# Kernel optimization log

Hardware: AMD Instinct MI355X
Metric: run time of the kernel (lower is better)

Reference implementation:

```python
import jax, jax.numpy as jnp
import numpy as np

D_MODEL = 512
N_HEADS = 8
DEPTH = D_MODEL // N_HEADS
NEG_INF = -1000000000.0


def setup_inputs() -> dict:
    key = jax.random.key(0)
    ks = jax.random.split(key, 12)
    B, S = 4, 2048
    scale = 0.02
    return {
        "Q": jax.random.normal(ks[0], (B, S, D_MODEL), jnp.float32),
        "K": jax.random.normal(ks[1], (B, S, D_MODEL), jnp.float32),
        "V": jax.random.normal(ks[2], (B, S, D_MODEL), jnp.float32),
        "mask": jax.random.randint(ks[3], (B, S, S), 0, 2, jnp.int32),
        "Wq": jax.random.normal(ks[4], (D_MODEL, D_MODEL), jnp.float32) * scale,
        "bq": jnp.zeros((D_MODEL,), jnp.float32),
        "Wk": jax.random.normal(ks[5], (D_MODEL, D_MODEL), jnp.float32) * scale,
        "bk": jnp.zeros((D_MODEL,), jnp.float32),
        "Wv": jax.random.normal(ks[6], (D_MODEL, D_MODEL), jnp.float32) * scale,
        "bv": jnp.zeros((D_MODEL,), jnp.float32),
        "Wo": jax.random.normal(ks[7], (D_MODEL, D_MODEL), jnp.float32) * scale,
        "bo": jnp.zeros((D_MODEL,), jnp.float32),
    }


def _split_heads(x, B):
    # [B, S, d_model] -> [B, H, S, depth]
    S = x.shape[1]
    return x.reshape(B, S, N_HEADS, DEPTH).transpose(0, 2, 1, 3)


def reference(Q, K, V, mask, Wq, bq, Wk, bk, Wv, bv, Wo, bo):
    B, S, _ = Q.shape
    q = _split_heads(Q @ Wq + bq, B)  # [B,H,S,d]
    k = _split_heads(K @ Wk + bk, B)
    v = _split_heads(V @ Wv + bv, B)
    scores = jnp.einsum("bhqd,bhkd->bhqk", q, k) / jnp.sqrt(
        jnp.asarray(DEPTH, jnp.float32))
    m = mask[:, None, :, :]  # broadcast over heads: [B,1,S,S]
    scores = jnp.where(m == 0, jnp.asarray(NEG_INF, scores.dtype), scores)
    attn = jax.nn.softmax(scores, axis=-1)
    ctx = jnp.einsum("bhqk,bhkd->bhqd", attn, v)
    ctx = ctx.transpose(0, 2, 1, 3).reshape(B, S, D_MODEL)
    return ctx @ Wo + bo
```

## Files before the change

kernel.cpp:

```cpp
#include <hip/hip_runtime.h>
#include <hip/hip_bf16.h>
#include <stdint.h>

typedef unsigned short u16;
typedef unsigned int u32;
typedef unsigned long long u64;
using bf16x8 = __attribute__((ext_vector_type(8))) __bf16;
using f32x4  = __attribute__((ext_vector_type(4))) float;
using f32x16 = __attribute__((ext_vector_type(16))) float;

static constexpr int B_ = 4, H_ = 8, S_ = 2048, D_ = 64, DM_ = 512;
#define QSCALE 0.1803368801111601f

__device__ __forceinline__ u16 f2b(float f) {
  u32 u = __float_as_uint(f);
  u = (u + 0x7FFFu + ((u >> 16) & 1u)) >> 16;
  return (u16)u;
}

__device__ __forceinline__ u32 cvtpk_bf16(float a, float b) {
  u32 r;
  asm("v_cvt_pk_bf16_f32 %0, %1, %2" : "=v"(r) : "v"(a), "v"(b));
  return r;
}
__device__ __forceinline__ void plswap(u32& a, u32& b) {
  asm("v_permlane32_swap_b32 %0, %1" : "+v"(a), "+v"(b));
}
__device__ __forceinline__ void gload16(const void* g, void* lds) {
  __builtin_amdgcn_global_load_lds(
      (const __attribute__((address_space(1))) u32*)g,
      (__attribute__((address_space(3))) u32*)lds, 16, 0, 0);
}
#if __has_builtin(__builtin_amdgcn_exp2f)
__device__ __forceinline__ float exp2fast(float x) { return __builtin_amdgcn_exp2f(x); }
#else
__device__ __forceinline__ float exp2fast(float x) {
  float r;
  asm("v_exp_f32 %0, %1" : "=v"(r) : "v"(x));
  return r;
}
#endif

__global__ __launch_bounds__(256) void prep_w_kernel(
    const float* __restrict__ Wq, const float* __restrict__ Wk,
    const float* __restrict__ Wv, const float* __restrict__ Wo,
    u16* __restrict__ Wtq, u16* __restrict__ Wtk, u16* __restrict__ Wtv, u16* __restrict__ Wto) {
  __shared__ float tile[32][33];
  const int z = blockIdx.z;
  const float* W = z == 0 ? Wq : z == 1 ? Wk : z == 2 ? Wv : Wo;
  u16* Wt       = z == 0 ? Wtq : z == 1 ? Wtk : z == 2 ? Wtv : Wto;
  const int k0 = blockIdx.x * 32, n0 = blockIdx.y * 32;
  const int t = threadIdx.x;
  {
    const int kl = t >> 3, nl4 = (t & 7) * 4;
    float4 v = *(const float4*)(W + (size_t)(k0 + kl) * DM_ + n0 + nl4);
    tile[kl][nl4 + 0] = v.x; tile[kl][nl4 + 1] = v.y;
    tile[kl][nl4 + 2] = v.z; tile[kl][nl4 + 3] = v.w;
  }
  __syncthreads();
  {
    const int nl = t >> 3, kl4 = (t & 7) * 4;
    ushort4 o;
    o.x = f2b(tile[kl4 + 0][nl]); o.y = f2b(tile[kl4 + 1][nl]);
    o.z = f2b(tile[kl4 + 2][nl]); o.w = f2b(tile[kl4 + 3][nl]);
    *(ushort4*)(Wt + (size_t)(n0 + nl) * DM_ + k0 + kl4) = o;
  }
}

__global__ void pack_mask_kernel(const int* __restrict__ mask, u32* __restrict__ bits) {
  int i = blockIdx.x * blockDim.x + threadIdx.x;
  unsigned long long bal = __ballot(mask[i] != 0);
  int lane = threadIdx.x & 63;
  if (lane == 0)       bits[i >> 5] = (u32)bal;
  else if (lane == 32) bits[i >> 5] = (u32)(bal >> 32);
}

__global__ __launch_bounds__(256) void gemm_qkv_kernel(
    const float* __restrict__ Qf, const float* __restrict__ Kf, const float* __restrict__ Vf,
    const u16* __restrict__ Wtq, const u16* __restrict__ Wtk, const u16* __restrict__ Wtv,
    const float* __restrict__ bq, const float* __restrict__ bk, const float* __restrict__ bv,
    u16* __restrict__ qp, u16* __restrict__ kp, u16* __restrict__ vp) {
  __shared__ u16 As[128][40];
  __shared__ u16 Bs[128][40];
  const int z = blockIdx.z;
  const float* A    = z == 0 ? Qf : z == 1 ? Kf : Vf;
  const u16* Bt     = z == 0 ? Wtq : z == 1 ? Wtk : Wtv;
  const float* bias = z == 0 ? bq : z == 1 ? bk : bv;
  u16* outp         = z == 0 ? qp : z == 1 ? kp : vp;
  const float scale = z == 0 ? QSCALE : 1.0f;

  const int t = threadIdx.x;
  const int lane = t & 63, wid = t >> 6;
  const int wr = wid >> 1, wc = wid & 1;
  const int l15 = lane & 15, l4 = lane >> 4;
  const int cn = blockIdx.x * 128, rm = blockIdx.y * 128;
  const int srow = t >> 2, scol = (t & 3) << 3;

  f32x4 acc[4][4] = {};

  for (int k0 = 0; k0 < DM_; k0 += 32) {
    __syncthreads();
    {
      const float* a0 = A + (size_t)(rm + srow) * DM_ + k0 + scol;
      float4 f0 = *(const float4*)a0, f1 = *(const float4*)(a0 + 4);
      uint4 u;
      u.x = cvtpk_bf16(f0.x, f0.y); u.y = cvtpk_bf16(f0.z, f0.w);
      u.z = cvtpk_bf16(f1.x, f1.y); u.w = cvtpk_bf16(f1.z, f1.w);
      *(uint4*)(&As[srow][scol]) = u;
      const float* a1 = A + (size_t)(rm + srow + 64) * DM_ + k0 + scol;
      float4 g0 = *(const float4*)a1, g1 = *(const float4*)(a1 + 4);
      uint4 w2;
      w2.x = cvtpk_bf16(g0.x, g0.y); w2.y = cvtpk_bf16(g0.z, g0.w);
      w2.z = cvtpk_bf16(g1.x, g1.y); w2.w = cvtpk_bf16(g1.z, g1.w);
      *(uint4*)(&As[srow + 64][scol]) = w2;
    }
    *(uint4*)(&Bs[srow][scol])      = *(const uint4*)(Bt + (size_t)(cn + srow) * DM_ + k0 + scol);
    *(uint4*)(&Bs[srow + 64][scol]) = *(const uint4*)(Bt + (size_t)(cn + srow + 64) * DM_ + k0 + scol);
    __syncthreads();
    bf16x8 af[4], bfr[4];
#pragma unroll
    for (int m = 0; m < 4; ++m)
      af[m] = *(const bf16x8*)(&As[wr * 64 + m * 16 + l15][l4 * 8]);
#pragma unroll
    for (int n = 0; n < 4; ++n)
      bfr[n] = *(const bf16x8*)(&Bs[wc * 64 + n * 16 + l15][l4 * 8]);
#pragma unroll
    for (int m = 0; m < 4; ++m)
#pragma unroll
      for (int n = 0; n < 4; ++n)
        acc[m][n] = __builtin_amdgcn_mfma_f32_16x16x32_bf16(af[m], bfr[n], acc[m][n], 0, 0, 0);
  }

#pragma unroll
  for (int m = 0; m < 4; ++m)
#pragma unroll
    for (int n = 0; n < 4; ++n) {
      int col = cn + wc * 64 + n * 16 + l15;
      float bv_ = bias[col];
#pragma unroll
      for (int r = 0; r < 4; ++r) {
        int row = rm + wr * 64 + m * 16 + l4 * 4 + r;
        float v = (acc[m][n][r] + bv_) * scale;
        int b = row >> 11, s = row & 2047;
        int h = col >> 6, d = col & 63;
        if (z < 2)
          outp[(((size_t)(b * H_ + h)) * S_ + s) * D_ + d] = f2b(v);
        else
          outp[(((size_t)(b * H_ + h)) * D_ + d) * S_ + s] = f2b(v);
      }
    }
}

__global__ __launch_bounds__(256) void gemm_out_kernel(
    const u16* __restrict__ A, const u16* __restrict__ Bt,
    const float* __restrict__ bias, float* __restrict__ outp) {
  __shared__ u16 As[64][40];
  __shared__ u16 Bs[128][40];
  const int t = threadIdx.x;
  const int lane = t & 63, w = t >> 6;
  const int l15 = lane & 15, l4 = lane >> 4;
  const int cn = blockIdx.x * 128, rm = blockIdx.y * 64;
  const int srow = t >> 2, scol = (t & 3) << 3;

  f32x4 acc[4][2] = {};

  for (int k0 = 0; k0 < DM_; k0 += 32) {
    __syncthreads();
    *(uint4*)(&As[srow][scol])      = *(const uint4*)(A + (size_t)(rm + srow) * DM_ + k0 + scol);
    *(uint4*)(&Bs[srow][scol])      = *(const uint4*)(Bt + (size_t)(cn + srow) * DM_ + k0 + scol);
    *(uint4*)(&Bs[srow + 64][scol]) = *(const uint4*)(Bt + (size_t)(cn + srow + 64) * DM_ + k0 + scol);
    __syncthreads();
    bf16x8 af[4], bfr[2];
#pragma unroll
    for (int m = 0; m < 4; ++m)
      af[m] = *(const bf16x8*)(&As[m * 16 + l15][l4 * 8]);
#pragma unroll
    for (int n = 0; n < 2; ++n)
      bfr[n] = *(const bf16x8*)(&Bs[w * 32 + n * 16 + l15][l4 * 8]);
#pragma unroll
    for (int m = 0; m < 4; ++m)
#pragma unroll
      for (int n = 0; n < 2; ++n)
        acc[m][n] = __builtin_amdgcn_mfma_f32_16x16x32_bf16(af[m], bfr[n], acc[m][n], 0, 0, 0);
  }

#pragma unroll
  for (int m = 0; m < 4; ++m)
#pragma unroll
    for (int n = 0; n < 2; ++n) {
      int col = cn + w * 32 + n * 16 + l15;
      float bv_ = bias[col];
#pragma unroll
      for (int r = 0; r < 4; ++r) {
        int row = rm + m * 16 + l4 * 4 + r;
        outp[(size_t)row * DM_ + col] = acc[m][n][r] + bv_;
      }
    }
}

__global__ __launch_bounds__(256) void attn_kernel(
    const u16* __restrict__ qp, const u16* __restrict__ kp, const u16* __restrict__ vp,
    const u64* __restrict__ mbits, u16* __restrict__ ctx) {
  __shared__ __align__(16) u16 Kl[2][64][64];
  __shared__ __align__(16) u16 Vl[2][64][64];
  const int t = threadIdx.x, lane = t & 63, w = t >> 6;
  const int l31 = lane & 31, hi = lane >> 5;
  const int wgid = blockIdx.x + 16 * (blockIdx.y + 8 * blockIdx.z);
  const int xcd = wgid & 7, idx = wgid >> 3;
  const int h = xcd, b = idx >> 4, qt = idx & 15;
  const size_t head  = ((size_t)(b * H_ + h)) * S_ * D_;
  const size_t headT = ((size_t)(b * H_ + h)) * D_ * S_;
  const int q0 = qt * 128 + w * 32;
  const int q  = q0 + l31;

  bf16x8 qf[4];
  {
    const u16* qrow = qp + head + (size_t)q * D_;
#pragma unroll
    for (int ks = 0; ks < 4; ++ks) qf[ks] = *(const bf16x8*)(qrow + ks * 16 + hi * 8);
  }

  const int kxor = (l31 & 7) << 4;
  const int rbase0 = l31 * 128, rbase1 = (32 + l31) * 128;
  int colx[4];
#pragma unroll
  for (int s = 0; s < 4; ++s) colx[s] = ((s * 32 + hi * 16) ^ kxor);

  const int srow = lane >> 3;
  const int scol = ((lane & 7) ^ srow) << 3;
  const int c0 = w, c1 = w + 4;
  const u16* ksrc0 = kp + head + (size_t)(c0 * 8 + srow) * D_ + scol;
  const u16* ksrc1 = kp + head + (size_t)(c1 * 8 + srow) * D_ + scol;
  const u16* vsrc0 = vp + headT + (size_t)(c0 * 8 + srow) * S_ + scol;
  const u16* vsrc1 = vp + headT + (size_t)(c1 * 8 + srow) * S_ + scol;

  f32x16 accO0, accO1;
#pragma unroll
  for (int i = 0; i < 16; ++i) { accO0[i] = 0.f; accO1[i] = 0.f; }
  float lrow = 0.f;

  const u64* mrowp = mbits + ((size_t)b * S_ + q) * (S_ / 64);

  auto stage = [&](int bufi, int kt) {
    char* kb = (char*)Kl + bufi * 8192;
    char* vb = (char*)Vl + bufi * 8192;
    gload16(ksrc0 + (size_t)kt * 4096, kb + c0 * 1024);
    gload16(ksrc1 + (size_t)kt * 4096, kb + c1 * 1024);
    gload16(vsrc0 + kt * 64, vb + c0 * 1024);
    gload16(vsrc1 + kt * 64, vb + c1 * 1024);
  };

  stage(0, 0);
  __syncthreads();
  int buf = 0;

  for (int kt = 0; kt < S_ / 64; ++kt) {
    if (kt < S_ / 64 - 1) stage(buf ^ 1, kt + 1);
    u64 mw = mrowp[kt] >> (hi * 4);
    const u32 mlo = (u32)mw, mhi = (u32)(mw >> 32);

    const char* kb = (const char*)Kl + buf * 8192;
    const char* vb = (const char*)Vl + buf * 8192;

    f32x16 s0, s1;
#pragma unroll
    for (int i = 0; i < 16; ++i) { s0[i] = 0.f; s1[i] = 0.f; }
    __builtin_amdgcn_s_setprio(1);
#pragma unroll
    for (int ks = 0; ks < 4; ++ks) {
      bf16x8 kf = *(const bf16x8*)(kb + rbase0 + colx[ks]);
      s0 = __builtin_amdgcn_mfma_f32_32x32x16_bf16(kf, qf[ks], s0, 0, 0, 0);
    }
#pragma unroll
    for (int ks = 0; ks < 4; ++ks) {
      bf16x8 kf = *(const bf16x8*)(kb + rbase1 + colx[ks]);
      s1 = __builtin_amdgcn_mfma_f32_32x32x16_bf16(kf, qf[ks], s1, 0, 0, 0);
    }
    __builtin_amdgcn_s_setprio(0);

    float e[32];
    float rs[4] = {0.f, 0.f, 0.f, 0.f};
#pragma unroll
    for (int c = 0; c < 2; ++c)
#pragma unroll
      for (int r = 0; r < 16; ++r) {
        const int kbit = c * 32 + (r & 3) + 8 * (r >> 2);
        const u32 wsel = (kbit < 32) ? mlo : mhi;
        float ex = exp2fast(c ? s1[r] : s0[r]);
        ex = ((wsel >> (kbit & 31)) & 1u) ? ex : 0.f;
        e[c * 16 + r] = ex;
        rs[r & 3] += ex;
      }
    float rsum = (rs[0] + rs[1]) + (rs[2] + rs[3]);
    rsum += __shfl_xor(rsum, 32);
    lrow += rsum;

#pragma unroll
    for (int c = 0; c < 2; ++c) {
      u32 pw[8];
#pragma unroll
      for (int j = 0; j < 8; ++j)
        pw[j] = cvtpk_bf16(e[c * 16 + 2 * j], e[c * 16 + 2 * j + 1]);
      plswap(pw[0], pw[2]); plswap(pw[1], pw[3]);
      plswap(pw[4], pw[6]); plswap(pw[5], pw[7]);
      __builtin_amdgcn_s_setprio(1);
#pragma unroll
      for (int s = 0; s < 2; ++s) {
        union { u32 wds[4]; bf16x8 v; } pa;
        pa.wds[0] = pw[s * 4 + 0]; pa.wds[1] = pw[s * 4 + 1];
        pa.wds[2] = pw[s * 4 + 2]; pa.wds[3] = pw[s * 4 + 3];
        const int slice = c * 2 + s;
        bf16x8 vf0 = *(const bf16x8*)(vb + rbase0 + colx[slice]);
        accO0 = __builtin_amdgcn_mfma_f32_32x32x16_bf16(pa.v, vf0, accO0, 0, 0, 0);
        bf16x8 vf1 = *(const bf16x8*)(vb + rbase1 + colx[slice]);
        accO1 = __builtin_amdgcn_mfma_f32_32x32x16_bf16(pa.v, vf1, accO1, 0, 0, 0);
      }
      __builtin_amdgcn_s_setprio(0);
    }
    __syncthreads();
    buf ^= 1;
  }

  float inv = 1.0f / lrow;
  float invr[16];
#pragma unroll
  for (int r = 0; r < 16; ++r) invr[r] = __shfl(inv, (r & 3) + 8 * (r >> 2) + 4 * hi);

  const int colA = h * 64 + l31, colB = h * 64 + 32 + l31;
#pragma unroll
  for (int r = 0; r < 16; ++r) {
    const int row = q0 + (r & 3) + 8 * (r >> 2) + 4 * hi;
    u16* o = ctx + ((size_t)(b * S_) + row) * DM_;
    o[colA] = f2b(accO0[r] * invr[r]);
    o[colB] = f2b(accO1[r] * invr[r]);
  }
}

extern "C" void kernel_launch(void* const* d_in, const int* in_sizes, int n_in,
                              void* d_out, int out_size, void* d_ws, size_t ws_size,
                              hipStream_t stream) {
  const float* Q  = (const float*)d_in[0];
  const float* K  = (const float*)d_in[1];
  const float* V  = (const float*)d_in[2];
  const int* mask = (const int*)d_in[3];
  const float* Wq = (const float*)d_in[4];
  const float* bq = (const float*)d_in[5];
  const float* Wk = (const float*)d_in[6];
  const float* bk = (const float*)d_in[7];
  const float* Wv = (const float*)d_in[8];
  const float* bv = (const float*)d_in[9];
  const float* Wo = (const float*)d_in[10];
  const float* bo = (const float*)d_in[11];

  char* ws = (char*)d_ws;
  size_t off = 0;
  auto alloc = [&](size_t bytes) -> void* {
    void* p = ws + off;
    off += (bytes + 255) & ~(size_t)255;
    return p;
  };
  const size_t act_b = (size_t)B_ * S_ * DM_ * 2;
  u16* Wtq = (u16*)alloc((size_t)DM_ * DM_ * 2);
  u16* Wtk = (u16*)alloc((size_t)DM_ * DM_ * 2);
  u16* Wtv = (u16*)alloc((size_t)DM_ * DM_ * 2);
  u16* Wto = (u16*)alloc((size_t)DM_ * DM_ * 2);
  u32* mbits = (u32*)alloc((size_t)B_ * S_ * (S_ / 32) * 4);
  u16* qp  = (u16*)alloc(act_b);
  u16* kp  = (u16*)alloc(act_b);
  u16* vp  = (u16*)alloc(act_b);
  u16* ctx = (u16*)alloc(act_b);

  prep_w_kernel<<<dim3(16, 16, 4), 256, 0, stream>>>(Wq, Wk, Wv, Wo, Wtq, Wtk, Wtv, Wto);
  pack_mask_kernel<<<(B_ * S_ * S_) / 256, 256, 0, stream>>>(mask, mbits);

  gemm_qkv_kernel<<<dim3(4, 64, 3), 256, 0, stream>>>(
      Q, K, V, Wtq, Wtk, Wtv, bq, bk, bv, qp, kp, vp);

  attn_kernel<<<dim3(16, 8, 4), 256, 0, stream>>>(qp, kp, vp, (const u64*)mbits, ctx);

  gemm_out_kernel<<<dim3(4, 128), 256, 0, stream>>>(ctx, Wto, bo, (float*)d_out);
}
```

Baseline: 151.0 us.

## Split keys across waves and load K/V directly from global memory

The attention kernel drops its double-buffered LDS staging of K/V tiles. It now splits each 64-query block into two query subtiles, each processed by two waves covering interleaved halves of the key range, and merges the partial outputs and row sums through LDS at the end. K and V fragments are read straight from global memory into registers. The grid doubles to 1024 blocks with an occupancy hint, to get more parallelism and remove the per-iteration barriers. In exchange, K/V are no longer shared through LDS across waves, so L2/global traffic per block goes up.

```diff
diff --git a/kernel.cpp b/kernel.cpp
--- a/kernel.cpp
+++ b/kernel.cpp
@@ -25,11 +25,6 @@
 }
 __device__ __forceinline__ void plswap(u32& a, u32& b) {
   asm("v_permlane32_swap_b32 %0, %1" : "+v"(a), "+v"(b));
-}
-__device__ __forceinline__ void gload16(const void* g, void* lds) {
-  __builtin_amdgcn_global_load_lds(
-      (const __attribute__((address_space(1))) u32*)g,
-      (__attribute__((address_space(3))) u32*)lds, 16, 0, 0);
 }
 #if __has_builtin(__builtin_amdgcn_exp2f)
 __device__ __forceinline__ float exp2fast(float x) { return __builtin_amdgcn_exp2f(x); }
@@ -198,19 +193,20 @@
     }
 }
 
-__global__ __launch_bounds__(256) void attn_kernel(
+__global__ __launch_bounds__(256, 4) void attn_kernel(
     const u16* __restrict__ qp, const u16* __restrict__ kp, const u16* __restrict__ vp,
     const u64* __restrict__ mbits, u16* __restrict__ ctx) {
-  __shared__ __align__(16) u16 Kl[2][64][64];
-  __shared__ __align__(16) u16 Vl[2][64][64];
+  __shared__ float Ol[2][32][64];
+  __shared__ float Ll[2][32];
   const int t = threadIdx.x, lane = t & 63, w = t >> 6;
   const int l31 = lane & 31, hi = lane >> 5;
-  const int wgid = blockIdx.x + 16 * (blockIdx.y + 8 * blockIdx.z);
-  const int xcd = wgid & 7, idx = wgid >> 3;
-  const int h = xcd, b = idx >> 4, qt = idx & 15;
+  const int qsub = w & 1, khalf = w >> 1;
+  const int wgid = blockIdx.x;
+  const int h = wgid & 7, idx = wgid >> 3;
+  const int b = idx >> 5, qt = idx & 31;
   const size_t head  = ((size_t)(b * H_ + h)) * S_ * D_;
   const size_t headT = ((size_t)(b * H_ + h)) * D_ * S_;
-  const int q0 = qt * 128 + w * 32;
+  const int q0 = qt * 64 + qsub * 32;
   const int q  = q0 + l31;
 
   bf16x8 qf[4];
@@ -220,63 +216,40 @@
     for (int ks = 0; ks < 4; ++ks) qf[ks] = *(const bf16x8*)(qrow + ks * 16 + hi * 8);
   }
 
-  const int kxor = (l31 & 7) << 4;
-  const int rbase0 = l31 * 128, rbase1 = (32 + l31) * 128;
-  int colx[4];
-#pragma unroll
-  for (int s = 0; s < 4; ++s) colx[s] = ((s * 32 + hi * 16) ^ kxor);
-
-  const int srow = lane >> 3;
-  const int scol = ((lane & 7) ^ srow) << 3;
-  const int c0 = w, c1 = w + 4;
-  const u16* ksrc0 = kp + head + (size_t)(c0 * 8 + srow) * D_ + scol;
-  const u16* ksrc1 = kp + head + (size_t)(c1 * 8 + srow) * D_ + scol;
-  const u16* vsrc0 = vp + headT + (size_t)(c0 * 8 + srow) * S_ + scol;
-  const u16* vsrc1 = vp + headT + (size_t)(c1 * 8 + srow) * S_ + scol;
+  const u16* kp0 = kp + head + ((size_t)khalf * 64 + l31) * D_ + hi * 8;
+  const u16* kp1 = kp0 + 32 * D_;
+  const u16* vp0 = vp + headT + (size_t)l31 * S_ + khalf * 64 + hi * 8;
+  const u16* vp1 = vp0 + (size_t)32 * S_;
+  const u64* mp  = mbits + ((size_t)b * S_ + q) * (S_ / 64) + khalf;
 
   f32x16 accO0, accO1;
 #pragma unroll
   for (int i = 0; i < 16; ++i) { accO0[i] = 0.f; accO1[i] = 0.f; }
   float lrow = 0.f;
 
-  const u64* mrowp = mbits + ((size_t)b * S_ + q) * (S_ / 64);
-
-  auto stage = [&](int bufi, int kt) {
-    char* kb = (char*)Kl + bufi * 8192;
-    char* vb = (char*)Vl + bufi * 8192;
-    gload16(ksrc0 + (size_t)kt * 4096, kb + c0 * 1024);
-    gload16(ksrc1 + (size_t)kt * 4096, kb + c1 * 1024);
-    gload16(vsrc0 + kt * 64, vb + c0 * 1024);
-    gload16(vsrc1 + kt * 64, vb + c1 * 1024);
-  };
-
-  stage(0, 0);
-  __syncthreads();
-  int buf = 0;
-
-  for (int kt = 0; kt < S_ / 64; ++kt) {
-    if (kt < S_ / 64 - 1) stage(buf ^ 1, kt + 1);
-    u64 mw = mrowp[kt] >> (hi * 4);
+  for (int it = 0; it < 16; ++it) {
+    u64 mw = mp[it * 2] >> (hi * 4);
     const u32 mlo = (u32)mw, mhi = (u32)(mw >> 32);
 
-    const char* kb = (const char*)Kl + buf * 8192;
-    const char* vb = (const char*)Vl + buf * 8192;
-
     f32x16 s0, s1;
 #pragma unroll
     for (int i = 0; i < 16; ++i) { s0[i] = 0.f; s1[i] = 0.f; }
-    __builtin_amdgcn_s_setprio(1);
-#pragma unroll
-    for (int ks = 0; ks < 4; ++ks) {
-      bf16x8 kf = *(const bf16x8*)(kb + rbase0 + colx[ks]);
-      s0 = __builtin_amdgcn_mfma_f32_32x32x16_bf16(kf, qf[ks], s0, 0, 0, 0);
-    }
-#pragma unroll
-    for (int ks = 0; ks < 4; ++ks) {
-      bf16x8 kf = *(const bf16x8*)(kb + rbase1 + colx[ks]);
-      s1 = __builtin_amdgcn_mfma_f32_32x32x16_bf16(kf, qf[ks], s1, 0, 0, 0);
-    }
-    __builtin_amdgcn_s_setprio(0);
+    {
+      bf16x8 kf0[4], kf1[4];
+#pragma unroll
+      for (int ks = 0; ks < 4; ++ks) kf0[ks] = *(const bf16x8*)(kp0 + ks * 16);
+#pragma unroll
+      for (int ks = 0; ks < 4; ++ks) kf1[ks] = *(const bf16x8*)(kp1 + ks * 16);
+      __builtin_amdgcn_s_setprio(1);
+#pragma unroll
+      for (int ks = 0; ks < 4; ++ks)
+        s0 = __builtin_amdgcn_mfma_f32_32x32x16_bf16(kf0[ks], qf[ks], s0, 0, 0, 0);
+#pragma unroll
+      for (int ks = 0; ks < 4; ++ks)
+        s1 = __builtin_amdgcn_mfma_f32_32x32x16_bf16(kf1[ks], qf[ks], s1, 0, 0, 0);
+      __builtin_amdgcn_s_setprio(0);
+    }
+    kp0 += 128 * D_; kp1 += 128 * D_;
 
     float e[32];
     float rs[4] = {0.f, 0.f, 0.f, 0.f};
@@ -303,36 +276,49 @@
         pw[j] = cvtpk_bf16(e[c * 16 + 2 * j], e[c * 16 + 2 * j + 1]);
       plswap(pw[0], pw[2]); plswap(pw[1], pw[3]);
       plswap(pw[4], pw[6]); plswap(pw[5], pw[7]);
-      __builtin_amdgcn_s_setprio(1);
 #pragma unroll
       for (int s = 0; s < 2; ++s) {
         union { u32 wds[4]; bf16x8 v; } pa;
         pa.wds[0] = pw[s * 4 + 0]; pa.wds[1] = pw[s * 4 + 1];
         pa.wds[2] = pw[s * 4 + 2]; pa.wds[3] = pw[s * 4 + 3];
         const int slice = c * 2 + s;
-        bf16x8 vf0 = *(const bf16x8*)(vb + rbase0 + colx[slice]);
+        bf16x8 vf0 = *(const bf16x8*)(vp0 + slice * 16);
+        bf16x8 vf1 = *(const bf16x8*)(vp1 + slice * 16);
+        __builtin_amdgcn_s_setprio(1);
         accO0 = __builtin_amdgcn_mfma_f32_32x32x16_bf16(pa.v, vf0, accO0, 0, 0, 0);
-        bf16x8 vf1 = *(const bf16x8*)(vb + rbase1 + colx[slice]);
         accO1 = __builtin_amdgcn_mfma_f32_32x32x16_bf16(pa.v, vf1, accO1, 0, 0, 0);
+        __builtin_amdgcn_s_setprio(0);
       }
-      __builtin_amdgcn_s_setprio(0);
-    }
-    __syncthreads();
-    buf ^= 1;
-  }
-
-  float inv = 1.0f / lrow;
-  float invr[16];
-#pragma unroll
-  for (int r = 0; r < 16; ++r) invr[r] = __shfl(inv, (r & 3) + 8 * (r >> 2) + 4 * hi);
-
-  const int colA = h * 64 + l31, colB = h * 64 + 32 + l31;
-#pragma unroll
-  for (int r = 0; r < 16; ++r) {
-    const int row = q0 + (r & 3) + 8 * (r >> 2) + 4 * hi;
-    u16* o = ctx + ((size_t)(b * S_) + row) * DM_;
-    o[colA] = f2b(accO0[r] * invr[r]);
-    o[colB] = f2b(accO1[r] * invr[r]);
+    }
+    vp0 += 128; vp1 += 128;
+  }
+
+  if (khalf == 1) {
+#pragma unroll
+    for (int r = 0; r < 16; ++r) {
+      const int qr = (r & 3) + 8 * (r >> 2) + 4 * hi;
+      Ol[qsub][qr][l31]      = accO0[r];
+      Ol[qsub][qr][32 + l31] = accO1[r];
+    }
+    if (hi == 0) Ll[qsub][l31] = lrow;
+  }
+  __syncthreads();
+  if (khalf == 0) {
+    lrow += Ll[qsub][l31];
+    float inv = 1.0f / lrow;
+    float invr[16];
+#pragma unroll
+    for (int r = 0; r < 16; ++r) invr[r] = __shfl(inv, (r & 3) + 8 * (r >> 2) + 4 * hi);
+
+    const int colA = h * 64 + l31, colB = h * 64 + 32 + l31;
+#pragma unroll
+    for (int r = 0; r < 16; ++r) {
+      const int qr = (r & 3) + 8 * (r >> 2) + 4 * hi;
+      const int row = q0 + qr;
+      u16* o = ctx + ((size_t)(b * S_) + row) * DM_;
+      o[colA] = f2b((accO0[r] + Ol[qsub][qr][l31])      * invr[r]);
+      o[colB] = f2b((accO1[r] + Ol[qsub][qr][32 + l31]) * invr[r]);
+    }
   }
 }
 
@@ -376,7 +362,7 @@
   gemm_qkv_kernel<<<dim3(4, 64, 3), 256, 0, stream>>>(
       Q, K, V, Wtq, Wtk, Wtv, bq, bk, bv, qp, kp, vp);
 
-  attn_kernel<<<dim3(16, 8, 4), 256, 0, stream>>>(qp, kp, vp, (const u64*)mbits, ctx);
+  attn_kernel<<<dim3(1024), 256, 0, stream>>>(qp, kp, vp, (const u64*)mbits, ctx);
 
   gemm_out_kernel<<<dim3(4, 128), 256, 0, stream>>>(ctx, Wto, bo, (float*)d_out);
 }
```

Result: slower. 214.8 us (+42.3%).

## Split key tiles across wave pairs in attention with LDS reduction of partials

Applied to the files above, without the earlier changes.

Each block now handles 64 queries instead of 128, with two waves per query group each processing half of every 64-key tile. The partial output accumulators and row sums from the second wave are combined through shared memory before normalization. The grid doubles to 1024 blocks and launch bounds request higher occupancy, aiming to fill the GPU better and shorten per-wave dependency chains. In exchange, K/V tiles are loaded per 64 queries rather than per 128, so global/LDS traffic per query rises, and an extra reduction epilogue is added.

```diff
diff --git a/kernel.cpp b/kernel.cpp
--- a/kernel.cpp
+++ b/kernel.cpp
@@ -198,19 +198,19 @@
     }
 }
 
-__global__ __launch_bounds__(256) void attn_kernel(
+__global__ __launch_bounds__(256, 4) void attn_kernel(
     const u16* __restrict__ qp, const u16* __restrict__ kp, const u16* __restrict__ vp,
     const u64* __restrict__ mbits, u16* __restrict__ ctx) {
-  __shared__ __align__(16) u16 Kl[2][64][64];
-  __shared__ __align__(16) u16 Vl[2][64][64];
+  __shared__ __align__(16) char smem[32768];
   const int t = threadIdx.x, lane = t & 63, w = t >> 6;
   const int l31 = lane & 31, hi = lane >> 5;
-  const int wgid = blockIdx.x + 16 * (blockIdx.y + 8 * blockIdx.z);
-  const int xcd = wgid & 7, idx = wgid >> 3;
-  const int h = xcd, b = idx >> 4, qt = idx & 15;
+  const int ksub = w & 1, qsub = w >> 1;
+  const int wgid = blockIdx.x;
+  const int h = wgid & 7, idx = wgid >> 3;
+  const int b = idx >> 5, qt = idx & 31;
   const size_t head  = ((size_t)(b * H_ + h)) * S_ * D_;
   const size_t headT = ((size_t)(b * H_ + h)) * D_ * S_;
-  const int q0 = qt * 128 + w * 32;
+  const int q0 = qt * 64 + qsub * 32;
   const int q  = q0 + l31;
 
   bf16x8 qf[4];
@@ -221,10 +221,14 @@
   }
 
   const int kxor = (l31 & 7) << 4;
+  const int krbase = (ksub * 32 + l31) * 128;
   const int rbase0 = l31 * 128, rbase1 = (32 + l31) * 128;
   int colx[4];
 #pragma unroll
   for (int s = 0; s < 4; ++s) colx[s] = ((s * 32 + hi * 16) ^ kxor);
+  int vcolx[2];
+#pragma unroll
+  for (int s = 0; s < 2; ++s) vcolx[s] = ((ksub * 64 + s * 32 + hi * 16) ^ kxor);
 
   const int srow = lane >> 3;
   const int scol = ((lane & 7) ^ srow) << 3;
@@ -242,8 +246,8 @@
   const u64* mrowp = mbits + ((size_t)b * S_ + q) * (S_ / 64);
 
   auto stage = [&](int bufi, int kt) {
-    char* kb = (char*)Kl + bufi * 8192;
-    char* vb = (char*)Vl + bufi * 8192;
+    char* kb = smem + bufi * 8192;
+    char* vb = smem + 16384 + bufi * 8192;
     gload16(ksrc0 + (size_t)kt * 4096, kb + c0 * 1024);
     gload16(ksrc1 + (size_t)kt * 4096, kb + c1 * 1024);
     gload16(vsrc0 + kt * 64, vb + c0 * 1024);
@@ -256,63 +260,55 @@
 
   for (int kt = 0; kt < S_ / 64; ++kt) {
     if (kt < S_ / 64 - 1) stage(buf ^ 1, kt + 1);
-    u64 mw = mrowp[kt] >> (hi * 4);
-    const u32 mlo = (u32)mw, mhi = (u32)(mw >> 32);
-
-    const char* kb = (const char*)Kl + buf * 8192;
-    const char* vb = (const char*)Vl + buf * 8192;
-
-    f32x16 s0, s1;
-#pragma unroll
-    for (int i = 0; i < 16; ++i) { s0[i] = 0.f; s1[i] = 0.f; }
-    __builtin_amdgcn_s_setprio(1);
-#pragma unroll
-    for (int ks = 0; ks < 4; ++ks) {
-      bf16x8 kf = *(const bf16x8*)(kb + rbase0 + colx[ks]);
-      s0 = __builtin_amdgcn_mfma_f32_32x32x16_bf16(kf, qf[ks], s0, 0, 0, 0);
-    }
-#pragma unroll
-    for (int ks = 0; ks < 4; ++ks) {
-      bf16x8 kf = *(const bf16x8*)(kb + rbase1 + colx[ks]);
-      s1 = __builtin_amdgcn_mfma_f32_32x32x16_bf16(kf, qf[ks], s1, 0, 0, 0);
-    }
-    __builtin_amdgcn_s_setprio(0);
-
-    float e[32];
+    const u32 m32 = (u32)(mrowp[kt] >> (ksub * 32 + hi * 4));
+
+    const char* kb = smem + buf * 8192;
+    const char* vb = smem + 16384 + buf * 8192;
+
+    f32x16 s;
+#pragma unroll
+    for (int i = 0; i < 16; ++i) s[i] = 0.f;
+    {
+      bf16x8 kf[4];
+#pragma unroll
+      for (int ks = 0; ks < 4; ++ks) kf[ks] = *(const bf16x8*)(kb + krbase + colx[ks]);
+      __builtin_amdgcn_s_setprio(1);
+#pragma unroll
+      for (int ks = 0; ks < 4; ++ks)
+        s = __builtin_amdgcn_mfma_f32_32x32x16_bf16(kf[ks], qf[ks], s, 0, 0, 0);
+      __builtin_amdgcn_s_setprio(0);
+    }
+
+    float e[16];
     float rs[4] = {0.f, 0.f, 0.f, 0.f};
 #pragma unroll
-    for (int c = 0; c < 2; ++c)
-#pragma unroll
-      for (int r = 0; r < 16; ++r) {
-        const int kbit = c * 32 + (r & 3) + 8 * (r >> 2);
-        const u32 wsel = (kbit < 32) ? mlo : mhi;
-        float ex = exp2fast(c ? s1[r] : s0[r]);
-        ex = ((wsel >> (kbit & 31)) & 1u) ? ex : 0.f;
-        e[c * 16 + r] = ex;
-        rs[r & 3] += ex;
-      }
+    for (int r = 0; r < 16; ++r) {
+      const int kbit = (r & 3) + 8 * (r >> 2);
+      float ex = exp2fast(s[r]);
+      ex = ((m32 >> kbit) & 1u) ? ex : 0.f;
+      e[r] = ex;
+      rs[r & 3] += ex;
+    }
     float rsum = (rs[0] + rs[1]) + (rs[2] + rs[3]);
     rsum += __shfl_xor(rsum, 32);
     lrow += rsum;
 
-#pragma unroll
-    for (int c = 0; c < 2; ++c) {
+    {
       u32 pw[8];
 #pragma unroll
       for (int j = 0; j < 8; ++j)
-        pw[j] = cvtpk_bf16(e[c * 16 + 2 * j], e[c * 16 + 2 * j + 1]);
+        pw[j] = cvtpk_bf16(e[2 * j], e[2 * j + 1]);
       plswap(pw[0], pw[2]); plswap(pw[1], pw[3]);
       plswap(pw[4], pw[6]); plswap(pw[5], pw[7]);
       __builtin_amdgcn_s_setprio(1);
 #pragma unroll
-      for (int s = 0; s < 2; ++s) {
+      for (int s2 = 0; s2 < 2; ++s2) {
         union { u32 wds[4]; bf16x8 v; } pa;
-        pa.wds[0] = pw[s * 4 + 0]; pa.wds[1] = pw[s * 4 + 1];
-        pa.wds[2] = pw[s * 4 + 2]; pa.wds[3] = pw[s * 4 + 3];
-        const int slice = c * 2 + s;
-        bf16x8 vf0 = *(const bf16x8*)(vb + rbase0 + colx[slice]);
+        pa.wds[0] = pw[s2 * 4 + 0]; pa.wds[1] = pw[s2 * 4 + 1];
+        pa.wds[2] = pw[s2 * 4 + 2]; pa.wds[3] = pw[s2 * 4 + 3];
+        bf16x8 vf0 = *(const bf16x8*)(vb + rbase0 + vcolx[s2]);
         accO0 = __builtin_amdgcn_mfma_f32_32x32x16_bf16(pa.v, vf0, accO0, 0, 0, 0);
-        bf16x8 vf1 = *(const bf16x8*)(vb + rbase1 + colx[slice]);
+        bf16x8 vf1 = *(const bf16x8*)(vb + rbase1 + vcolx[s2]);
         accO1 = __builtin_amdgcn_mfma_f32_32x32x16_bf16(pa.v, vf1, accO1, 0, 0, 0);
       }
       __builtin_amdgcn_s_setprio(0);
@@ -321,18 +317,34 @@
     buf ^= 1;
   }
 
-  float inv = 1.0f / lrow;
-  float invr[16];
-#pragma unroll
-  for (int r = 0; r < 16; ++r) invr[r] = __shfl(inv, (r & 3) + 8 * (r >> 2) + 4 * hi);
-
-  const int colA = h * 64 + l31, colB = h * 64 + 32 + l31;
-#pragma unroll
-  for (int r = 0; r < 16; ++r) {
-    const int row = q0 + (r & 3) + 8 * (r >> 2) + 4 * hi;
-    u16* o = ctx + ((size_t)(b * S_) + row) * DM_;
-    o[colA] = f2b(accO0[r] * invr[r]);
-    o[colB] = f2b(accO1[r] * invr[r]);
+  float (*Ol)[32][64] = (float (*)[32][64])smem;
+  float* Ll = (float*)(smem + 16384);
+  if (ksub == 1) {
+#pragma unroll
+    for (int r = 0; r < 16; ++r) {
+      const int qr = (r & 3) + 8 * (r >> 2) + 4 * hi;
+      Ol[qsub][qr][l31]      = accO0[r];
+      Ol[qsub][qr][32 + l31] = accO1[r];
+    }
+    if (hi == 0) Ll[qsub * 32 + l31] = lrow;
+  }
+  __syncthreads();
+  if (ksub == 0) {
+    lrow += Ll[qsub * 32 + l31];
+    float inv = 1.0f / lrow;
+    float invr[16];
+#pragma unroll
+    for (int r = 0; r < 16; ++r) invr[r] = __shfl(inv, (r & 3) + 8 * (r >> 2) + 4 * hi);
+
+    const int colA = h * 64 + l31, colB = h * 64 + 32 + l31;
+#pragma unroll
+    for (int r = 0; r < 16; ++r) {
+      const int qr = (r & 3) + 8 * (r >> 2) + 4 * hi;
+      const int row = q0 + qr;
+      u16* o = ctx + ((size_t)(b * S_) + row) * DM_;
+      o[colA] = f2b((accO0[r] + Ol[qsub][qr][l31])      * invr[r]);
+      o[colB] = f2b((accO1[r] + Ol[qsub][qr][32 + l31]) * invr[r]);
+    }
   }
 }
 
@@ -376,7 +388,7 @@
   gemm_qkv_kernel<<<dim3(4, 64, 3), 256, 0, stream>>>(
       Q, K, V, Wtq, Wtk, Wtv, bq, bk, bv, qp, kp, vp);
 
-  attn_kernel<<<dim3(16, 8, 4), 256, 0, stream>>>(qp, kp, vp, (const u64*)mbits, ctx);
+  attn_kernel<<<dim3(1024), 256, 0, stream>>>(qp, kp, vp, (const u64*)mbits, ctx);
 
   gemm_out_kernel<<<dim3(4, 128), 256, 0, stream>>>(ctx, Wto, bo, (float*)d_out);
 }
```

Result: faster. 146.6 us (-2.9%).
